# Performance work log

Measured on AMD Instinct MI355X. Metric: run time of the kernel, lower is better.

## Reference

```python
import jax, jax.numpy as jnp
import numpy as np

B, T, D, H = 4, 2048, 1024, 16
DK = D // H

def setup_inputs() -> dict:
    key = jax.random.key(0)
    k1, k2, k3 = jax.random.split(key, 3)
    x = jax.random.normal(k1, (B, T, D), dtype=jnp.float32)
    w_qkv = jax.random.normal(k2, (D, 3 * D), dtype=jnp.float32) * (1.0 / np.sqrt(D))
    w_proj = jax.random.normal(k3, (D, D), dtype=jnp.float32) * (1.0 / np.sqrt(D))
    # additive causal mask: 0 on/below diagonal, -inf above
    neg = jnp.finfo(jnp.float32).min
    attn_mask = jnp.where(jnp.tril(jnp.ones((T, T), dtype=bool)), 0.0, neg)[None, None]
    return {"x": x, "attn_mask": attn_mask, "w_qkv": w_qkv, "w_proj": w_proj}


def reference(x, attn_mask, w_qkv, w_proj):
    Bx, Tx, Dx = x.shape
    qkv = x @ w_qkv                                  # [B,T,3D]
    q, k, v = jnp.split(qkv, 3, axis=-1)
    # [B,T,D] -> [B,H,T,dk]
    def to_heads(t):
        return t.reshape(Bx, Tx, H, DK).transpose(0, 2, 1, 3)
    q, k, v = to_heads(q), to_heads(k), to_heads(v)
    attn = jnp.einsum("bhqd,bhkd->bhqk", q, k) / jnp.sqrt(jnp.float32(DK))
    attn = attn + attn_mask
    attn = jax.nn.softmax(attn, axis=-1)
    out = jnp.einsum("bhqk,bhkd->bhqd", attn, v)     # [B,H,T,dk]
    out = out.transpose(0, 2, 1, 3).reshape(Bx, Tx, Dx)
    return out @ w_proj
```

## Files before the change

kernel.cpp:

```cpp
#include <hip/hip_runtime.h>
#include <hip/hip_bf16.h>
#include <stdint.h>

typedef __bf16 bf16x8 __attribute__((ext_vector_type(8)));
typedef __bf16 bf16x4 __attribute__((ext_vector_type(4)));
typedef float  f32x4  __attribute__((ext_vector_type(4)));

__device__ __forceinline__ void gl_lds16(const void* g, void* l) {
  __builtin_amdgcn_global_load_lds(
      (const __attribute__((address_space(1))) unsigned int*)g,
      (__attribute__((address_space(3))) unsigned int*)l, 16, 0, 0);
}

__global__ __launch_bounds__(256) void prep_kernel(
    const float* __restrict__ x, __bf16* __restrict__ Xb,
    const float* __restrict__ w_qkv, __bf16* __restrict__ wt_qkv,
    const float* __restrict__ w_proj, __bf16* __restrict__ wt_proj) {
  __shared__ __bf16 tile[64][65];
  const int bid = blockIdx.x, t = threadIdx.x;
  if (bid < 4096) {
    const size_t i = ((size_t)bid * 256 + t) * 8;
    float4 v0 = *reinterpret_cast<const float4*>(x + i);
    float4 v1 = *reinterpret_cast<const float4*>(x + i + 4);
    bf16x8 o;
    o[0] = (__bf16)v0.x; o[1] = (__bf16)v0.y; o[2] = (__bf16)v0.z; o[3] = (__bf16)v0.w;
    o[4] = (__bf16)v1.x; o[5] = (__bf16)v1.y; o[6] = (__bf16)v1.z; o[7] = (__bf16)v1.w;
    *reinterpret_cast<bf16x8*>(Xb + i) = o;
    return;
  }
  const float* src; __bf16* dst; int K, N, bx, by;
  if (bid < 4864) {
    int idx = bid - 4096;
    src = w_qkv; dst = wt_qkv; K = 1024; N = 3072;
    bx = idx % 48; by = idx / 48;
  } else {
    int idx = bid - 4864;
    src = w_proj; dst = wt_proj; K = 1024; N = 1024;
    bx = idx & 15; by = idx >> 4;
  }
  const int n0 = bx * 64, k0 = by * 64;
#pragma unroll
  for (int e = 0; e < 16; ++e) {
    int idx = e * 256 + t;
    int kk = idx >> 6, nn = idx & 63;
    tile[nn][kk] = (__bf16)src[(size_t)(k0 + kk) * N + n0 + nn];
  }
  __syncthreads();
#pragma unroll
  for (int e = 0; e < 16; ++e) {
    int idx = e * 256 + t;
    int nn = idx >> 6, kk = idx & 63;
    dst[(size_t)(n0 + nn) * K + k0 + kk] = tile[nn][kk];
  }
}

template <int NFRAG>
__device__ __forceinline__ void gemm_core_1024(
    const __bf16* __restrict__ Ag, const __bf16* __restrict__ Bg,
    int m0, int n0, __bf16* lds, f32x4 (&acc)[8][NFRAG]) {
  constexpr int BUFSZ = 4096 + NFRAG * 2048;
  const int tid = threadIdx.x;
  const int wv = tid >> 6, l = tid & 63, g = l >> 4, lr = l & 15;
  const int sswL = (lr & 3) ^ ((lr >> 2) & 3);

  int arow[2], acol[2], brow[NFRAG], bcol[NFRAG];
#pragma unroll
  for (int e = 0; e < 2; ++e) {
    int c = e * 256 + tid, row = c >> 2, slot = c & 3;
    arow[e] = row;
    acol[e] = (slot ^ ((row & 3) ^ ((row >> 2) & 3))) * 8;
  }
#pragma unroll
  for (int e = 0; e < NFRAG; ++e) {
    int c = e * 256 + tid, row = c >> 2, slot = c & 3;
    brow[e] = row;
    bcol[e] = (slot ^ ((row & 3) ^ ((row >> 2) & 3))) * 8;
  }

  auto STAGE = [&](int bufb, int t) {
    const int kb = t * 32;
#pragma unroll
    for (int e = 0; e < 2; ++e)
      gl_lds16(Ag + (size_t)(m0 + arow[e]) * 1024 + kb + acol[e],
               lds + bufb + (e * 256 + wv * 64) * 8);
#pragma unroll
    for (int e = 0; e < NFRAG; ++e)
      gl_lds16(Bg + (size_t)(n0 + brow[e]) * 1024 + kb + bcol[e],
               lds + bufb + 4096 + (e * 256 + wv * 64) * 8);
  };

  int cur = 0, nx = BUFSZ, nn = 2 * BUFSZ;
  STAGE(cur, 0);
  STAGE(nx, 1);

#pragma unroll 1
  for (int t = 0; t < 32; ++t) {
    if (t < 31) {
      if constexpr (NFRAG == 3) asm volatile("s_waitcnt vmcnt(5)" ::: "memory");
      else                      asm volatile("s_waitcnt vmcnt(4)" ::: "memory");
    } else {
      asm volatile("s_waitcnt vmcnt(0)" ::: "memory");
    }
    __builtin_amdgcn_s_barrier();
    __builtin_amdgcn_sched_barrier(0);
    if (t + 2 < 32) STAGE(nn, t + 2);

    const char* Ab = (const char*)(lds + cur);
    const char* Bb = (const char*)(lds + cur + 4096);
    bf16x8 a[8], b[NFRAG];
#pragma unroll
    for (int mf = 0; mf < 8; ++mf)
      a[mf] = *reinterpret_cast<const bf16x8*>(
          Ab + (mf * 16 + lr) * 64 + ((g ^ sswL) << 4));
#pragma unroll
    for (int nf = 0; nf < NFRAG; ++nf)
      b[nf] = *reinterpret_cast<const bf16x8*>(
          Bb + (wv * NFRAG * 16 + nf * 16 + lr) * 64 + ((g ^ sswL) << 4));
    __builtin_amdgcn_s_setprio(1);
#pragma unroll
    for (int mf = 0; mf < 8; ++mf)
#pragma unroll
      for (int nf = 0; nf < NFRAG; ++nf)
        acc[mf][nf] = __builtin_amdgcn_mfma_f32_16x16x32_bf16(
            a[mf], b[nf], acc[mf][nf], 0, 0, 0);
    __builtin_amdgcn_s_setprio(0);

    int tmp = cur; cur = nx; nx = nn; nn = tmp;
  }
}

__global__ __launch_bounds__(256, 2) void qkv_gemm(
    const __bf16* __restrict__ Xb, const __bf16* __restrict__ WT,
    __bf16* __restrict__ Qb, __bf16* __restrict__ Kb, __bf16* __restrict__ Vb) {
  __shared__ __bf16 lds[30720];
  const int lin = blockIdx.x;
  const int sw = (lin & 7) * 128 + (lin >> 3);
  const int rb = sw >> 4, cb = sw & 15;
  const int m0 = rb * 128, n0 = cb * 192;

  f32x4 acc[8][3] = {};
  gemm_core_1024<3>(Xb, WT, m0, n0, lds, acc);

  const int tid = threadIdx.x, wv = tid >> 6, l = tid & 63, g = l >> 4, lr = l & 15;
#pragma unroll
  for (int mf = 0; mf < 8; ++mf)
#pragma unroll
    for (int nf = 0; nf < 3; ++nf) {
      int m_ = m0 + mf * 16 + g * 4;
      int nb = n0 + wv * 48 + nf * 16;
      int which = nb >> 10, hc = nb & 1023;
      int hh = hc >> 6, dk0 = hc & 63;
      int bbv = m_ >> 11, tt = m_ & 2047;
      if (which == 2) {
        bf16x4 vk;
        vk[0] = (__bf16)acc[mf][nf][0]; vk[1] = (__bf16)acc[mf][nf][1];
        vk[2] = (__bf16)acc[mf][nf][2]; vk[3] = (__bf16)acc[mf][nf][3];
        *reinterpret_cast<bf16x4*>(
            &Vb[((size_t)(bbv * 16 + hh) * 64 + dk0 + lr) * 2048 + tt]) = vk;
      } else if (which == 0) {
#pragma unroll
        for (int j = 0; j < 4; ++j)
          Qb[(((size_t)(bbv * 16 + hh)) * 2048 + tt + j) * 64 + dk0 + lr] =
              (__bf16)(acc[mf][nf][j] * 0.18033688f);
      } else {
#pragma unroll
        for (int j = 0; j < 4; ++j)
          Kb[(((size_t)(bbv * 16 + hh)) * 2048 + tt + j) * 64 + dk0 + lr] =
              (__bf16)acc[mf][nf][j];
      }
    }
}

__global__ __launch_bounds__(256, 2) void proj_gemm(
    const __bf16* __restrict__ A, const __bf16* __restrict__ WT,
    float* __restrict__ Out) {
  __shared__ __bf16 lds[24576];
  const int lin = blockIdx.x;
  const int sw = (lin & 7) * 64 + (lin >> 3);
  const int rb = sw >> 3, cb = sw & 7;
  const int m0 = rb * 128, n0 = cb * 128;

  f32x4 acc[8][2] = {};
  gemm_core_1024<2>(A, WT, m0, n0, lds, acc);

  const int tid = threadIdx.x, wv = tid >> 6, l = tid & 63, g = l >> 4, lr = l & 15;
#pragma unroll
  for (int mf = 0; mf < 8; ++mf)
#pragma unroll
    for (int nf = 0; nf < 2; ++nf) {
      int m_ = m0 + mf * 16 + g * 4;
      int n  = n0 + wv * 32 + nf * 16 + lr;
#pragma unroll
      for (int j = 0; j < 4; ++j)
        Out[(size_t)(m_ + j) * 1024 + n] = acc[mf][nf][j];
    }
}

__global__ __launch_bounds__(256, 2) void attn_kernel(
    const __bf16* __restrict__ Qb, const __bf16* __restrict__ Kb,
    const __bf16* __restrict__ VTb, __bf16* __restrict__ Ob) {
  __shared__ __bf16 Ks[2][4096];
  __shared__ __bf16 Vs[2][4096];
  __shared__ __bf16 PlA[4][1024];
  __shared__ __bf16 PlB[4][1024];
  const int t = threadIdx.x, l = t & 63, w = t >> 6;
  const int g = l >> 4, lr = l & 15;
  const int bid = blockIdx.x;
  const int logical = (bid & 7) * 64 + (bid >> 3);
  const int pj = logical & 7, bh = logical >> 3;
  const int bb = bh >> 4, h = bh & 15;
  const __bf16* Kbase = Kb  + (size_t)bh * 2048 * 64;
  const __bf16* Vbase = VTb + (size_t)bh * 64 * 2048;
  const __bf16* Qbase = Qb  + (size_t)bh * 2048 * 64;
  const int swz = (lr & 7) << 4;

  int cur = 0;
#pragma unroll 1
  for (int phase = 0; phase < 2; ++phase) {
    const int J = phase ? (15 - pj) : pj;
    const int qtA = 2 * J, qtB = 2 * J + 1;
    const int qrowA = J * 128 + w * 16 + lr;
    const int qrowB = qrowA + 64;
    const bf16x8 qfA0 = *reinterpret_cast<const bf16x8*>(Qbase + (size_t)qrowA * 64 + g * 8);
    const bf16x8 qfA1 = *reinterpret_cast<const bf16x8*>(Qbase + (size_t)qrowA * 64 + 32 + g * 8);
    const bf16x8 qfB0 = *reinterpret_cast<const bf16x8*>(Qbase + (size_t)qrowB * 64 + g * 8);
    const bf16x8 qfB1 = *reinterpret_cast<const bf16x8*>(Qbase + (size_t)qrowB * 64 + 32 + g * 8);

    f32x4 otA[4] = {}, otB[4] = {};
    float lsA = 0.f, lsB = 0.f;

#pragma unroll
    for (int rep = 0; rep < 2; ++rep) {
      int c = w * 128 + rep * 64 + l;
      int row = c >> 3, cc = c & 7;
      int pc = (cc ^ (row & 7)) * 8;
      gl_lds16(Kbase + (size_t)row * 64 + pc, &Ks[cur][(w * 128 + rep * 64) * 8]);
      gl_lds16(Vbase + (size_t)row * 2048 + pc, &Vs[cur][(w * 128 + rep * 64) * 8]);
    }
    __syncthreads();

    for (int kt = 0; kt <= qtB; ++kt) {
      const bool aAct = (kt <= qtA);
      if (kt < qtB) {
        const int nv0 = (kt + 1) * 64;
#pragma unroll
        for (int rep = 0; rep < 2; ++rep) {
          int c = w * 128 + rep * 64 + l;
          int row = c >> 3, cc = c & 7;
          int pc = (cc ^ (row & 7)) * 8;
          gl_lds16(Kbase + (size_t)(nv0 + row) * 64 + pc,
                   &Ks[cur ^ 1][(w * 128 + rep * 64) * 8]);
          gl_lds16(Vbase + (size_t)row * 2048 + nv0 + pc,
                   &Vs[cur ^ 1][(w * 128 + rep * 64) * 8]);
        }
      }
      bf16x8 klo[4], khi[4];
#pragma unroll
      for (int nf = 0; nf < 4; ++nf) {
        const char* kr = (const char*)&Ks[cur][(nf * 16 + lr) * 64];
        klo[nf] = *reinterpret_cast<const bf16x8*>(kr + ((g * 16) ^ swz));
        khi[nf] = *reinterpret_cast<const bf16x8*>(kr + ((64 + g * 16) ^ swz));
      }
      f32x4 stA[4], stB[4];
      __builtin_amdgcn_s_setprio(1);
#pragma unroll
      for (int nf = 0; nf < 4; ++nf) {
        f32x4 z = {};
        z = __builtin_amdgcn_mfma_f32_16x16x32_bf16(klo[nf], qfB0, z, 0, 0, 0);
        stB[nf] = __builtin_amdgcn_mfma_f32_16x16x32_bf16(khi[nf], qfB1, z, 0, 0, 0);
      }
      if (aAct) {
#pragma unroll
        for (int nf = 0; nf < 4; ++nf) {
          f32x4 z = {};
          z = __builtin_amdgcn_mfma_f32_16x16x32_bf16(klo[nf], qfA0, z, 0, 0, 0);
          stA[nf] = __builtin_amdgcn_mfma_f32_16x16x32_bf16(khi[nf], qfA1, z, 0, 0, 0);
        }
      }
      __builtin_amdgcn_s_setprio(0);
      if (kt == qtB) {
#pragma unroll
        for (int nf = 0; nf < 4; ++nf)
#pragma unroll
          for (int j = 0; j < 4; ++j)
            if (nf * 16 + g * 4 + j > w * 16 + lr) stB[nf][j] = -INFINITY;
      }
      if (aAct && kt == qtA) {
#pragma unroll
        for (int nf = 0; nf < 4; ++nf)
#pragma unroll
          for (int j = 0; j < 4; ++j)
            if (nf * 16 + g * 4 + j > w * 16 + lr) stA[nf][j] = -INFINITY;
      }
      {
        float rs = 0.f;
        char* prow = (char*)&PlB[w][lr * 64];
#pragma unroll
        for (int nf = 0; nf < 4; ++nf) {
#pragma unroll
          for (int j = 0; j < 4; ++j) {
            float p = __builtin_amdgcn_exp2f(stB[nf][j]);
            stB[nf][j] = p;
            rs += p;
          }
          bf16x4 pk;
          pk[0] = (__bf16)stB[nf][0]; pk[1] = (__bf16)stB[nf][1];
          pk[2] = (__bf16)stB[nf][2]; pk[3] = (__bf16)stB[nf][3];
          *reinterpret_cast<bf16x4*>(prow + ((nf * 32 + g * 8) ^ swz)) = pk;
        }
        lsB += rs;
      }
      if (aAct) {
        float rs = 0.f;
        char* prow = (char*)&PlA[w][lr * 64];
#pragma unroll
        for (int nf = 0; nf < 4; ++nf) {
#pragma unroll
          for (int j = 0; j < 4; ++j) {
            float p = __builtin_amdgcn_exp2f(stA[nf][j]);
            stA[nf][j] = p;
            rs += p;
          }
          bf16x4 pk;
          pk[0] = (__bf16)stA[nf][0]; pk[1] = (__bf16)stA[nf][1];
          pk[2] = (__bf16)stA[nf][2]; pk[3] = (__bf16)stA[nf][3];
          *reinterpret_cast<bf16x4*>(prow + ((nf * 32 + g * 8) ^ swz)) = pk;
        }
        lsA += rs;
      }
      {
        bf16x8 vlo[4], vhi[4];
#pragma unroll
        for (int nf = 0; nf < 4; ++nf) {
          const char* vr = (const char*)&Vs[cur][(nf * 16 + lr) * 64];
          vlo[nf] = *reinterpret_cast<const bf16x8*>(vr + ((g * 16) ^ swz));
          vhi[nf] = *reinterpret_cast<const bf16x8*>(vr + ((64 + g * 16) ^ swz));
        }
        const char* prB = (const char*)&PlB[w][lr * 64];
        bf16x8 pb0 = *reinterpret_cast<const bf16x8*>(prB + ((g * 16) ^ swz));
        bf16x8 pb1 = *reinterpret_cast<const bf16x8*>(prB + ((64 + g * 16) ^ swz));
        __builtin_amdgcn_s_setprio(1);
#pragma unroll
        for (int nf = 0; nf < 4; ++nf) {
          otB[nf] = __builtin_amdgcn_mfma_f32_16x16x32_bf16(vlo[nf], pb0, otB[nf], 0, 0, 0);
          otB[nf] = __builtin_amdgcn_mfma_f32_16x16x32_bf16(vhi[nf], pb1, otB[nf], 0, 0, 0);
        }
        __builtin_amdgcn_s_setprio(0);
        if (aAct) {
          const char* prA = (const char*)&PlA[w][lr * 64];
          bf16x8 pa0 = *reinterpret_cast<const bf16x8*>(prA + ((g * 16) ^ swz));
          bf16x8 pa1 = *reinterpret_cast<const bf16x8*>(prA + ((64 + g * 16) ^ swz));
          __builtin_amdgcn_s_setprio(1);
#pragma unroll
          for (int nf = 0; nf < 4; ++nf) {
            otA[nf] = __builtin_amdgcn_mfma_f32_16x16x32_bf16(vlo[nf], pa0, otA[nf], 0, 0, 0);
            otA[nf] = __builtin_amdgcn_mfma_f32_16x16x32_bf16(vhi[nf], pa1, otA[nf], 0, 0, 0);
          }
          __builtin_amdgcn_s_setprio(0);
        }
      }
      __syncthreads();
      cur ^= 1;
    }

    lsA += __shfl_xor(lsA, 16); lsA += __shfl_xor(lsA, 32);
    lsB += __shfl_xor(lsB, 16); lsB += __shfl_xor(lsB, 32);
    const float rlA = 1.f / lsA, rlB = 1.f / lsB;
#pragma unroll
    for (int nf = 0; nf < 4; ++nf) {
      bf16x4 ok;
      ok[0] = (__bf16)(otA[nf][0] * rlA); ok[1] = (__bf16)(otA[nf][1] * rlA);
      ok[2] = (__bf16)(otA[nf][2] * rlA); ok[3] = (__bf16)(otA[nf][3] * rlA);
      *reinterpret_cast<bf16x4*>(
          &Ob[((size_t)(bb * 2048 + qrowA)) * 1024 + h * 64 + nf * 16 + g * 4]) = ok;
      bf16x4 ok2;
      ok2[0] = (__bf16)(otB[nf][0] * rlB); ok2[1] = (__bf16)(otB[nf][1] * rlB);
      ok2[2] = (__bf16)(otB[nf][2] * rlB); ok2[3] = (__bf16)(otB[nf][3] * rlB);
      *reinterpret_cast<bf16x4*>(
          &Ob[((size_t)(bb * 2048 + qrowB)) * 1024 + h * 64 + nf * 16 + g * 4]) = ok2;
    }
  }
}

extern "C" void kernel_launch(void* const* d_in, const int* in_sizes, int n_in,
                              void* d_out, int out_size, void* d_ws, size_t ws_size,
                              hipStream_t stream) {
  const float* x      = (const float*)d_in[0];
  const float* w_qkv  = (const float*)d_in[2];
  const float* w_proj = (const float*)d_in[3];
  float* out = (float*)d_out;

  char* ws = (char*)d_ws;
  __bf16* wt_qkv  = (__bf16*)(ws);
  __bf16* wt_proj = (__bf16*)(ws + 6291456);
  __bf16* Qb      = (__bf16*)(ws + 8388608);
  __bf16* Kb      = (__bf16*)(ws + 8388608 + 16777216);
  __bf16* VTb     = (__bf16*)(ws + 8388608 + 2 * 16777216);
  __bf16* Ob      = (__bf16*)(ws + 8388608 + 3 * 16777216);
  __bf16* Xb      = Ob;

  prep_kernel<<<5120, 256, 0, stream>>>(x, Xb, w_qkv, wt_qkv, w_proj, wt_proj);
  qkv_gemm<<<1024, 256, 0, stream>>>(Xb, wt_qkv, Qb, Kb, VTb);
  attn_kernel<<<512, 256, 0, stream>>>(Qb, Kb, VTb, Ob);
  proj_gemm<<<512, 256, 0, stream>>>(Ob, wt_proj, out);
}
```

Baseline: 159.6 us.

## Switch QKV and projection GEMMs to 256x256 tiles with 8 waves

Replaces the 128-row GEMM core with a 256x256 block tile computed by 512 threads arranged as 2x4 waves, with a new LDS swizzle and triple buffering. The B-tile prefetch is split to issue between the two MFMA halves, with extra barriers. Larger tiles raise arithmetic intensity and cut global loads per FLOP. The cost is far fewer blocks (384 and 128), one block per CU, and possible load imbalance and lower occupancy.

```diff
diff --git a/kernel.cpp b/kernel.cpp
--- a/kernel.cpp
+++ b/kernel.cpp
@@ -54,142 +54,142 @@
   }
 }
 
-template <int NFRAG>
-__device__ __forceinline__ void gemm_core_1024(
-    const __bf16* __restrict__ Ag, const __bf16* __restrict__ Bg,
-    int m0, int n0, __bf16* lds, f32x4 (&acc)[8][NFRAG]) {
-  constexpr int BUFSZ = 4096 + NFRAG * 2048;
-  const int tid = threadIdx.x;
-  const int wv = tid >> 6, l = tid & 63, g = l >> 4, lr = l & 15;
-  const int sswL = (lr & 3) ^ ((lr >> 2) & 3);
-
-  int arow[2], acol[2], brow[NFRAG], bcol[NFRAG];
-#pragma unroll
-  for (int e = 0; e < 2; ++e) {
-    int c = e * 256 + tid, row = c >> 2, slot = c & 3;
-    arow[e] = row;
-    acol[e] = (slot ^ ((row & 3) ^ ((row >> 2) & 3))) * 8;
-  }
-#pragma unroll
-  for (int e = 0; e < NFRAG; ++e) {
-    int c = e * 256 + tid, row = c >> 2, slot = c & 3;
-    brow[e] = row;
-    bcol[e] = (slot ^ ((row & 3) ^ ((row >> 2) & 3))) * 8;
-  }
-
-  auto STAGE = [&](int bufb, int t) {
-    const int kb = t * 32;
-#pragma unroll
-    for (int e = 0; e < 2; ++e)
-      gl_lds16(Ag + (size_t)(m0 + arow[e]) * 1024 + kb + acol[e],
-               lds + bufb + (e * 256 + wv * 64) * 8);
-#pragma unroll
-    for (int e = 0; e < NFRAG; ++e)
-      gl_lds16(Bg + (size_t)(n0 + brow[e]) * 1024 + kb + bcol[e],
-               lds + bufb + 4096 + (e * 256 + wv * 64) * 8);
-  };
-
-  int cur = 0, nx = BUFSZ, nn = 2 * BUFSZ;
-  STAGE(cur, 0);
-  STAGE(nx, 1);
-
-#pragma unroll 1
-  for (int t = 0; t < 32; ++t) {
-    if (t < 31) {
-      if constexpr (NFRAG == 3) asm volatile("s_waitcnt vmcnt(5)" ::: "memory");
-      else                      asm volatile("s_waitcnt vmcnt(4)" ::: "memory");
-    } else {
-      asm volatile("s_waitcnt vmcnt(0)" ::: "memory");
-    }
-    __builtin_amdgcn_s_barrier();
-    __builtin_amdgcn_sched_barrier(0);
-    if (t + 2 < 32) STAGE(nn, t + 2);
-
-    const char* Ab = (const char*)(lds + cur);
-    const char* Bb = (const char*)(lds + cur + 4096);
-    bf16x8 a[8], b[NFRAG];
-#pragma unroll
-    for (int mf = 0; mf < 8; ++mf)
-      a[mf] = *reinterpret_cast<const bf16x8*>(
-          Ab + (mf * 16 + lr) * 64 + ((g ^ sswL) << 4));
-#pragma unroll
-    for (int nf = 0; nf < NFRAG; ++nf)
-      b[nf] = *reinterpret_cast<const bf16x8*>(
-          Bb + (wv * NFRAG * 16 + nf * 16 + lr) * 64 + ((g ^ sswL) << 4));
-    __builtin_amdgcn_s_setprio(1);
-#pragma unroll
-    for (int mf = 0; mf < 8; ++mf)
-#pragma unroll
-      for (int nf = 0; nf < NFRAG; ++nf)
-        acc[mf][nf] = __builtin_amdgcn_mfma_f32_16x16x32_bf16(
-            a[mf], b[nf], acc[mf][nf], 0, 0, 0);
-    __builtin_amdgcn_s_setprio(0);
-
-    int tmp = cur; cur = nx; nx = nn; nn = tmp;
-  }
-}
-
-__global__ __launch_bounds__(256, 2) void qkv_gemm(
+#define GEMM256_CORE(Ag, Bg, m0, n0, lds, acc)                                  \
+  const int tid = threadIdx.x;                                                  \
+  const int wv = tid >> 6, l = tid & 63, g = l >> 4, lr = l & 15;               \
+  const int wm = wv >> 2, wn = wv & 3;                                          \
+  int srow[2], scol[2];                                                         \
+  _Pragma("unroll")                                                             \
+  for (int e = 0; e < 2; ++e) {                                                 \
+    int c = e * 512 + tid;                                                      \
+    int row = c >> 2, slot = c & 3;                                             \
+    srow[e] = row;                                                              \
+    scol[e] = (slot ^ ((row >> 1) & 3)) * 8;                                    \
+  }                                                                             \
+  const int sdst0 = tid * 8;                                                    \
+  auto STAGE_A = [&](int buf, int t) {                                          \
+    const int kb = t * 32;                                                      \
+    _Pragma("unroll")                                                           \
+    for (int e = 0; e < 2; ++e)                                                 \
+      gl_lds16(Ag + (size_t)(m0 + srow[e]) * 1024 + kb + scol[e],               \
+               lds + buf * 16384 + e * 4096 + sdst0);                           \
+  };                                                                            \
+  auto STAGE_B = [&](int buf, int t) {                                          \
+    const int kb = t * 32;                                                      \
+    _Pragma("unroll")                                                           \
+    for (int e = 0; e < 2; ++e)                                                 \
+      gl_lds16(Bg + (size_t)(n0 + srow[e]) * 1024 + kb + scol[e],               \
+               lds + buf * 16384 + 8192 + e * 4096 + sdst0);                    \
+  };                                                                            \
+  const int swb = (g ^ ((lr >> 1) & 3)) * 8;                                    \
+  const int arow0 = wm * 128 + lr;                                              \
+  const int brow0 = wn * 64 + lr;                                               \
+  STAGE_A(0, 0); STAGE_B(0, 0);                                                 \
+  STAGE_A(1, 1); STAGE_B(1, 1);                                                 \
+  int bt = 0;                                                                   \
+  _Pragma("unroll 1")                                                           \
+  for (int t = 0; t < 32; ++t) {                                                \
+    if (t < 31) asm volatile("s_waitcnt vmcnt(4)" ::: "memory");                \
+    else        asm volatile("s_waitcnt vmcnt(0)" ::: "memory");                \
+    __builtin_amdgcn_s_barrier();                                               \
+    __builtin_amdgcn_sched_barrier(0);                                          \
+    const __bf16* Ab = lds + bt * 16384;                                        \
+    const __bf16* Bb = Ab + 8192;                                               \
+    const int bs = (bt + 2 >= 3) ? (bt - 1) : (bt + 2);                         \
+    bf16x8 a[8], b[4];                                                          \
+    if (t + 2 < 32) STAGE_A(bs, t + 2);                                         \
+    _Pragma("unroll")                                                           \
+    for (int mf = 0; mf < 4; ++mf)                                              \
+      a[mf] = *reinterpret_cast<const bf16x8*>(Ab + (arow0 + mf * 16) * 32 + swb); \
+    _Pragma("unroll")                                                           \
+    for (int nf = 0; nf < 4; ++nf)                                              \
+      b[nf] = *reinterpret_cast<const bf16x8*>(Bb + (brow0 + nf * 16) * 32 + swb); \
+    __builtin_amdgcn_s_barrier();                                               \
+    __builtin_amdgcn_s_setprio(1);                                              \
+    _Pragma("unroll")                                                           \
+    for (int mf = 0; mf < 4; ++mf)                                              \
+      _Pragma("unroll")                                                         \
+      for (int nf = 0; nf < 4; ++nf)                                            \
+        acc[mf][nf] = __builtin_amdgcn_mfma_f32_16x16x32_bf16(                  \
+            a[mf], b[nf], acc[mf][nf], 0, 0, 0);                                \
+    __builtin_amdgcn_s_setprio(0);                                              \
+    __builtin_amdgcn_sched_barrier(0);                                          \
+    if (t + 2 < 32) STAGE_B(bs, t + 2);                                         \
+    _Pragma("unroll")                                                           \
+    for (int mf = 4; mf < 8; ++mf)                                              \
+      a[mf] = *reinterpret_cast<const bf16x8*>(Ab + (arow0 + mf * 16) * 32 + swb); \
+    __builtin_amdgcn_s_barrier();                                               \
+    __builtin_amdgcn_s_setprio(1);                                              \
+    _Pragma("unroll")                                                           \
+    for (int mf = 4; mf < 8; ++mf)                                              \
+      _Pragma("unroll")                                                         \
+      for (int nf = 0; nf < 4; ++nf)                                            \
+        acc[mf][nf] = __builtin_amdgcn_mfma_f32_16x16x32_bf16(                  \
+            a[mf], b[nf], acc[mf][nf], 0, 0, 0);                                \
+    __builtin_amdgcn_s_setprio(0);                                              \
+    __builtin_amdgcn_sched_barrier(0);                                          \
+    bt = (bt + 1 == 3) ? 0 : bt + 1;                                            \
+  }
+
+__global__ __launch_bounds__(512, 1) void qkv_gemm(
     const __bf16* __restrict__ Xb, const __bf16* __restrict__ WT,
     __bf16* __restrict__ Qb, __bf16* __restrict__ Kb, __bf16* __restrict__ Vb) {
-  __shared__ __bf16 lds[30720];
+  __shared__ __bf16 lds[49152];
   const int lin = blockIdx.x;
-  const int sw = (lin & 7) * 128 + (lin >> 3);
-  const int rb = sw >> 4, cb = sw & 15;
-  const int m0 = rb * 128, n0 = cb * 192;
-
-  f32x4 acc[8][3] = {};
-  gemm_core_1024<3>(Xb, WT, m0, n0, lds, acc);
-
-  const int tid = threadIdx.x, wv = tid >> 6, l = tid & 63, g = l >> 4, lr = l & 15;
+  const int sw = (lin & 7) * 48 + (lin >> 3);
+  const int rb = sw / 12, cb = sw % 12;
+  const int m0 = rb * 256, n0 = cb * 256;
+
+  f32x4 acc[8][4] = {};
+  GEMM256_CORE(Xb, WT, m0, n0, lds, acc)
+
+  const int which = cb >> 2;
 #pragma unroll
   for (int mf = 0; mf < 8; ++mf)
 #pragma unroll
-    for (int nf = 0; nf < 3; ++nf) {
-      int m_ = m0 + mf * 16 + g * 4;
-      int nb = n0 + wv * 48 + nf * 16;
-      int which = nb >> 10, hc = nb & 1023;
-      int hh = hc >> 6, dk0 = hc & 63;
+    for (int nf = 0; nf < 4; ++nf) {
+      int m_ = m0 + wm * 128 + mf * 16 + g * 4;
+      int n  = n0 + wn * 64 + nf * 16 + lr;
+      int hc = n & 1023, hh = hc >> 6, dk = hc & 63;
       int bbv = m_ >> 11, tt = m_ & 2047;
       if (which == 2) {
         bf16x4 vk;
         vk[0] = (__bf16)acc[mf][nf][0]; vk[1] = (__bf16)acc[mf][nf][1];
         vk[2] = (__bf16)acc[mf][nf][2]; vk[3] = (__bf16)acc[mf][nf][3];
         *reinterpret_cast<bf16x4*>(
-            &Vb[((size_t)(bbv * 16 + hh) * 64 + dk0 + lr) * 2048 + tt]) = vk;
+            &Vb[((size_t)(bbv * 16 + hh) * 64 + dk) * 2048 + tt]) = vk;
       } else if (which == 0) {
 #pragma unroll
         for (int j = 0; j < 4; ++j)
-          Qb[(((size_t)(bbv * 16 + hh)) * 2048 + tt + j) * 64 + dk0 + lr] =
+          Qb[(((size_t)(bbv * 16 + hh)) * 2048 + tt + j) * 64 + dk] =
               (__bf16)(acc[mf][nf][j] * 0.18033688f);
       } else {
 #pragma unroll
         for (int j = 0; j < 4; ++j)
-          Kb[(((size_t)(bbv * 16 + hh)) * 2048 + tt + j) * 64 + dk0 + lr] =
+          Kb[(((size_t)(bbv * 16 + hh)) * 2048 + tt + j) * 64 + dk] =
               (__bf16)acc[mf][nf][j];
       }
     }
 }
 
-__global__ __launch_bounds__(256, 2) void proj_gemm(
+__global__ __launch_bounds__(512, 1) void proj_gemm(
     const __bf16* __restrict__ A, const __bf16* __restrict__ WT,
     float* __restrict__ Out) {
-  __shared__ __bf16 lds[24576];
+  __shared__ __bf16 lds[49152];
   const int lin = blockIdx.x;
-  const int sw = (lin & 7) * 64 + (lin >> 3);
-  const int rb = sw >> 3, cb = sw & 7;
-  const int m0 = rb * 128, n0 = cb * 128;
-
-  f32x4 acc[8][2] = {};
-  gemm_core_1024<2>(A, WT, m0, n0, lds, acc);
-
-  const int tid = threadIdx.x, wv = tid >> 6, l = tid & 63, g = l >> 4, lr = l & 15;
+  const int sw = (lin & 7) * 16 + (lin >> 3);
+  const int rb = sw >> 2, cb = sw & 3;
+  const int m0 = rb * 256, n0 = cb * 256;
+
+  f32x4 acc[8][4] = {};
+  GEMM256_CORE(A, WT, m0, n0, lds, acc)
+
 #pragma unroll
   for (int mf = 0; mf < 8; ++mf)
 #pragma unroll
-    for (int nf = 0; nf < 2; ++nf) {
-      int m_ = m0 + mf * 16 + g * 4;
-      int n  = n0 + wv * 32 + nf * 16 + lr;
+    for (int nf = 0; nf < 4; ++nf) {
+      int m_ = m0 + wm * 128 + mf * 16 + g * 4;
+      int n  = n0 + wn * 64 + nf * 16 + lr;
 #pragma unroll
       for (int j = 0; j < 4; ++j)
         Out[(size_t)(m_ + j) * 1024 + n] = acc[mf][nf][j];
@@ -400,7 +400,7 @@
   __bf16* Xb      = Ob;
 
   prep_kernel<<<5120, 256, 0, stream>>>(x, Xb, w_qkv, wt_qkv, w_proj, wt_proj);
-  qkv_gemm<<<1024, 256, 0, stream>>>(Xb, wt_qkv, Qb, Kb, VTb);
+  qkv_gemm<<<384, 512, 0, stream>>>(Xb, wt_qkv, Qb, Kb, VTb);
   attn_kernel<<<512, 256, 0, stream>>>(Qb, Kb, VTb, Ob);
-  proj_gemm<<<512, 256, 0, stream>>>(Ob, wt_proj, out);
-}
+  proj_gemm<<<128, 512, 0, stream>>>(Ob, wt_proj, out);
+}
```

New measurement: 170.0 us. 6.5% more time.

## Rewrite QKV GEMM with 256x256 tiles, 8 waves, and interleaved staging

Applied to the files above, without the earlier changes.

The QKV projection GEMM moves from 128x192 tiles with 4 waves to 256x256 tiles with 8 waves (2x4 wave grid) and 384 blocks. Loads are issued half-tile at a time and interleaved with the MFMA phases under a two-buffer LDS scheme with its own XOR swizzle. The aim is more data reuse per LDS byte and fewer global loads. The shared gemm_core read swizzle expression is also changed, which affects proj_gemm and risks a mismatch with how that core stages data if sswL was computed differently.

```diff
diff --git a/kernel.cpp b/kernel.cpp
--- a/kernel.cpp
+++ b/kernel.cpp
@@ -111,11 +111,11 @@
 #pragma unroll
     for (int mf = 0; mf < 8; ++mf)
       a[mf] = *reinterpret_cast<const bf16x8*>(
-          Ab + (mf * 16 + lr) * 64 + ((g ^ sswL) << 4));
+          Ab + (mf * 16 + lr) * 64 + (((lr & 3) ^ ((lr >> 2) & 3) ^ g) << 4));
 #pragma unroll
     for (int nf = 0; nf < NFRAG; ++nf)
       b[nf] = *reinterpret_cast<const bf16x8*>(
-          Bb + (wv * NFRAG * 16 + nf * 16 + lr) * 64 + ((g ^ sswL) << 4));
+          Bb + (wv * NFRAG * 16 + nf * 16 + lr) * 64 + (((lr & 3) ^ ((lr >> 2) & 3) ^ g) << 4));
     __builtin_amdgcn_s_setprio(1);
 #pragma unroll
     for (int mf = 0; mf < 8; ++mf)
@@ -129,43 +129,108 @@
   }
 }
 
-__global__ __launch_bounds__(256, 2) void qkv_gemm(
+__global__ __launch_bounds__(512, 2) void qkv_gemm(
     const __bf16* __restrict__ Xb, const __bf16* __restrict__ WT,
     __bf16* __restrict__ Qb, __bf16* __restrict__ Kb, __bf16* __restrict__ Vb) {
-  __shared__ __bf16 lds[30720];
+  __shared__ __bf16 lds[32768];
+  const int tid = threadIdx.x;
+  const int wv = tid >> 6, l = tid & 63, g = l >> 4, lr = l & 15;
+  const int wm = wv >> 2, wn = wv & 3;
   const int lin = blockIdx.x;
-  const int sw = (lin & 7) * 128 + (lin >> 3);
-  const int rb = sw >> 4, cb = sw & 15;
-  const int m0 = rb * 128, n0 = cb * 192;
-
-  f32x4 acc[8][3] = {};
-  gemm_core_1024<3>(Xb, WT, m0, n0, lds, acc);
-
-  const int tid = threadIdx.x, wv = tid >> 6, l = tid & 63, g = l >> 4, lr = l & 15;
+  const int sw = (lin & 7) * 48 + (lin >> 3);
+  const int rb = sw / 12, cb = sw % 12;
+  const int m0 = rb * 256, n0 = cb * 256;
+
+  const int strow = tid >> 2;
+  const int stcol = ((tid & 3) ^ ((strow >> 1) & 3)) * 8;
+
+  auto STAGE2 = [&](int tile, int isB) {
+    if (tile >= 32) return;
+    const __bf16* G = isB ? WT : Xb;
+    const int gr0 = isB ? n0 : m0;
+    __bf16* dst = lds + (isB ? 16384 : 0) + (tile & 1) * 8192;
+#pragma unroll
+    for (int h = 0; h < 2; ++h)
+      gl_lds16(G + (size_t)(gr0 + h * 128 + strow) * 1024 + tile * 32 + stcol,
+               dst + h * 4096 + tid * 8);
+  };
+
+  f32x4 acc[8][4] = {};
+
+  STAGE2(0, 1); STAGE2(0, 0); STAGE2(1, 1);
+  asm volatile("s_waitcnt vmcnt(2)" ::: "memory");
+  __builtin_amdgcn_s_barrier();
+
+  bf16x8 b[4];
+#pragma unroll 1
+  for (int i = 0; i < 16; ++i) {
+    const int t0 = 2 * i;
+#pragma unroll
+    for (int p = 0; p < 4; ++p) {
+      const int kt = p >> 1, mh = p & 1;
+      bf16x8 a[4];
+#pragma unroll
+      for (int m4 = 0; m4 < 4; ++m4) {
+        int r = wm * 128 + (mh * 4 + m4) * 16 + lr;
+        int sl = (g ^ ((r >> 1) & 3)) * 8;
+        a[m4] = *reinterpret_cast<const bf16x8*>(lds + kt * 8192 + r * 32 + sl);
+      }
+      if (mh == 0) {
+#pragma unroll
+        for (int nf = 0; nf < 4; ++nf) {
+          int r = wn * 64 + nf * 16 + lr;
+          int sl = (g ^ ((r >> 1) & 3)) * 8;
+          b[nf] = *reinterpret_cast<const bf16x8*>(lds + 16384 + kt * 8192 + r * 32 + sl);
+        }
+      }
+      if (p == 0) STAGE2(t0 + 1, 0);
+      if (p == 1) STAGE2(t0 + 2, 1);
+      if (p == 2) STAGE2(t0 + 2, 0);
+      if (p == 3) STAGE2(t0 + 3, 1);
+      __builtin_amdgcn_s_barrier();
+      asm volatile("s_waitcnt lgkmcnt(0)" ::: "memory");
+      __builtin_amdgcn_sched_barrier(0);
+      __builtin_amdgcn_s_setprio(1);
+#pragma unroll
+      for (int m4 = 0; m4 < 4; ++m4)
+#pragma unroll
+        for (int nf = 0; nf < 4; ++nf)
+          acc[mh * 4 + m4][nf] = __builtin_amdgcn_mfma_f32_16x16x32_bf16(
+              a[m4], b[nf], acc[mh * 4 + m4][nf], 0, 0, 0);
+      __builtin_amdgcn_s_setprio(0);
+      __builtin_amdgcn_sched_barrier(0);
+      if (p == 1 || p == 3) {
+        if (i < 15) asm volatile("s_waitcnt vmcnt(2)" ::: "memory");
+        else        asm volatile("s_waitcnt vmcnt(0)" ::: "memory");
+      }
+      __builtin_amdgcn_s_barrier();
+    }
+  }
+
+  const int which = cb >> 2;
 #pragma unroll
   for (int mf = 0; mf < 8; ++mf)
 #pragma unroll
-    for (int nf = 0; nf < 3; ++nf) {
-      int m_ = m0 + mf * 16 + g * 4;
-      int nb = n0 + wv * 48 + nf * 16;
-      int which = nb >> 10, hc = nb & 1023;
-      int hh = hc >> 6, dk0 = hc & 63;
+    for (int nf = 0; nf < 4; ++nf) {
+      int m_ = m0 + wm * 128 + mf * 16 + g * 4;
+      int n  = n0 + wn * 64 + nf * 16 + lr;
+      int hc = n & 1023, hh = hc >> 6, dk = hc & 63;
       int bbv = m_ >> 11, tt = m_ & 2047;
       if (which == 2) {
         bf16x4 vk;
         vk[0] = (__bf16)acc[mf][nf][0]; vk[1] = (__bf16)acc[mf][nf][1];
         vk[2] = (__bf16)acc[mf][nf][2]; vk[3] = (__bf16)acc[mf][nf][3];
         *reinterpret_cast<bf16x4*>(
-            &Vb[((size_t)(bbv * 16 + hh) * 64 + dk0 + lr) * 2048 + tt]) = vk;
+            &Vb[((size_t)(bbv * 16 + hh) * 64 + dk) * 2048 + tt]) = vk;
       } else if (which == 0) {
 #pragma unroll
         for (int j = 0; j < 4; ++j)
-          Qb[(((size_t)(bbv * 16 + hh)) * 2048 + tt + j) * 64 + dk0 + lr] =
+          Qb[(((size_t)(bbv * 16 + hh)) * 2048 + tt + j) * 64 + dk] =
               (__bf16)(acc[mf][nf][j] * 0.18033688f);
       } else {
 #pragma unroll
         for (int j = 0; j < 4; ++j)
-          Kb[(((size_t)(bbv * 16 + hh)) * 2048 + tt + j) * 64 + dk0 + lr] =
+          Kb[(((size_t)(bbv * 16 + hh)) * 2048 + tt + j) * 64 + dk] =
               (__bf16)acc[mf][nf][j];
       }
     }
@@ -400,7 +465,7 @@
   __bf16* Xb      = Ob;
 
   prep_kernel<<<5120, 256, 0, stream>>>(x, Xb, w_qkv, wt_qkv, w_proj, wt_proj);
-  qkv_gemm<<<1024, 256, 0, stream>>>(Xb, wt_qkv, Qb, Kb, VTb);
+  qkv_gemm<<<384, 512, 0, stream>>>(Xb, wt_qkv, Qb, Kb, VTb);
   attn_kernel<<<512, 256, 0, stream>>>(Qb, Kb, VTb, Ob);
   proj_gemm<<<512, 256, 0, stream>>>(Ob, wt_proj, out);
 }
```

Measured after the change: 161.9 us. No clear change (+1.4%).

## Use 2x2 wave tiling with 128x128 tiles and four-stage LDS pipeline in GEMMs

Applied to the files above, without the earlier changes.

Replaces the GEMM core with a uniform 128x128 block tile in which the four waves form a 2x2 grid, each owning a 64x64 sub-tile, instead of every wave reading all 128 A rows. The loads now cycle through four LDS buffers three stages ahead, and fragment reads are issued before the next stage's global loads. This is meant to cut per-wave LDS fragment reads and hide more global latency. The QKV GEMM moves from 128x192 tiles to 128x128 (1536 blocks). The cost is more LDS per block (64 KB), which may limit occupancy.

```diff
diff --git a/kernel.cpp b/kernel.cpp
--- a/kernel.cpp
+++ b/kernel.cpp
@@ -54,118 +54,114 @@
   }
 }
 
-template <int NFRAG>
-__device__ __forceinline__ void gemm_core_1024(
+__device__ __forceinline__ void gemm128_core(
     const __bf16* __restrict__ Ag, const __bf16* __restrict__ Bg,
-    int m0, int n0, __bf16* lds, f32x4 (&acc)[8][NFRAG]) {
-  constexpr int BUFSZ = 4096 + NFRAG * 2048;
+    int m0, int n0, __bf16* lds, f32x4 (&acc)[4][4]) {
   const int tid = threadIdx.x;
   const int wv = tid >> 6, l = tid & 63, g = l >> 4, lr = l & 15;
-  const int sswL = (lr & 3) ^ ((lr >> 2) & 3);
-
-  int arow[2], acol[2], brow[NFRAG], bcol[NFRAG];
+  const int wm = wv >> 1, wn = wv & 1;
+
+  int srow[2], scolG[2];
 #pragma unroll
   for (int e = 0; e < 2; ++e) {
-    int c = e * 256 + tid, row = c >> 2, slot = c & 3;
-    arow[e] = row;
-    acol[e] = (slot ^ ((row & 3) ^ ((row >> 2) & 3))) * 8;
-  }
-#pragma unroll
-  for (int e = 0; e < NFRAG; ++e) {
-    int c = e * 256 + tid, row = c >> 2, slot = c & 3;
-    brow[e] = row;
-    bcol[e] = (slot ^ ((row & 3) ^ ((row >> 2) & 3))) * 8;
-  }
-
-  auto STAGE = [&](int bufb, int t) {
-    const int kb = t * 32;
-#pragma unroll
-    for (int e = 0; e < 2; ++e)
-      gl_lds16(Ag + (size_t)(m0 + arow[e]) * 1024 + kb + acol[e],
-               lds + bufb + (e * 256 + wv * 64) * 8);
-#pragma unroll
-    for (int e = 0; e < NFRAG; ++e)
-      gl_lds16(Bg + (size_t)(n0 + brow[e]) * 1024 + kb + bcol[e],
-               lds + bufb + 4096 + (e * 256 + wv * 64) * 8);
+    int linear = e * 256 + tid;
+    int row = linear >> 2, slotP = linear & 3;
+    srow[e] = row;
+    scolG[e] = (slotP ^ (row & 3) ^ ((row >> 2) & 3)) * 8;
+  }
+
+  auto STAGE = [&](int t) {
+    if (t >= 32) return;
+    const int bufO = (t & 3) * 8192;
+    const int kg = t * 32;
+#pragma unroll
+    for (int e = 0; e < 2; ++e) {
+      gl_lds16(Ag + (size_t)(m0 + srow[e]) * 1024 + kg + scolG[e],
+               lds + bufO + (e * 256 + tid) * 8);
+      gl_lds16(Bg + (size_t)(n0 + srow[e]) * 1024 + kg + scolG[e],
+               lds + bufO + 4096 + (e * 256 + tid) * 8);
+    }
   };
 
-  int cur = 0, nx = BUFSZ, nn = 2 * BUFSZ;
-  STAGE(cur, 0);
-  STAGE(nx, 1);
+  const int sl8 = (g ^ (lr & 3) ^ ((lr >> 2) & 3)) * 8;
+  const int arow0 = wm * 64 + lr;
+  const int brow0 = wn * 64 + lr;
+
+  STAGE(0); STAGE(1); STAGE(2);
 
 #pragma unroll 1
   for (int t = 0; t < 32; ++t) {
-    if (t < 31) {
-      if constexpr (NFRAG == 3) asm volatile("s_waitcnt vmcnt(5)" ::: "memory");
-      else                      asm volatile("s_waitcnt vmcnt(4)" ::: "memory");
-    } else {
-      asm volatile("s_waitcnt vmcnt(0)" ::: "memory");
-    }
+    if (t < 30)       asm volatile("s_waitcnt vmcnt(8)" ::: "memory");
+    else if (t == 30) asm volatile("s_waitcnt vmcnt(4)" ::: "memory");
+    else              asm volatile("s_waitcnt vmcnt(0)" ::: "memory");
     __builtin_amdgcn_s_barrier();
     __builtin_amdgcn_sched_barrier(0);
-    if (t + 2 < 32) STAGE(nn, t + 2);
-
-    const char* Ab = (const char*)(lds + cur);
-    const char* Bb = (const char*)(lds + cur + 4096);
-    bf16x8 a[8], b[NFRAG];
-#pragma unroll
-    for (int mf = 0; mf < 8; ++mf)
-      a[mf] = *reinterpret_cast<const bf16x8*>(
-          Ab + (mf * 16 + lr) * 64 + ((g ^ sswL) << 4));
-#pragma unroll
-    for (int nf = 0; nf < NFRAG; ++nf)
-      b[nf] = *reinterpret_cast<const bf16x8*>(
-          Bb + (wv * NFRAG * 16 + nf * 16 + lr) * 64 + ((g ^ sswL) << 4));
+
+    const __bf16* buf = lds + (t & 3) * 8192;
+    bf16x8 a[4], b[4];
+#pragma unroll
+    for (int mf = 0; mf < 4; ++mf)
+      a[mf] = *reinterpret_cast<const bf16x8*>(buf + (arow0 + mf * 16) * 32 + sl8);
+#pragma unroll
+    for (int nf = 0; nf < 4; ++nf)
+      b[nf] = *reinterpret_cast<const bf16x8*>(buf + 4096 + (brow0 + nf * 16) * 32 + sl8);
+
+    STAGE(t + 3);
+
+    asm volatile("s_waitcnt lgkmcnt(0)" ::: "memory");
+    __builtin_amdgcn_sched_barrier(0);
     __builtin_amdgcn_s_setprio(1);
 #pragma unroll
-    for (int mf = 0; mf < 8; ++mf)
-#pragma unroll
-      for (int nf = 0; nf < NFRAG; ++nf)
+    for (int mf = 0; mf < 4; ++mf)
+#pragma unroll
+      for (int nf = 0; nf < 4; ++nf)
         acc[mf][nf] = __builtin_amdgcn_mfma_f32_16x16x32_bf16(
             a[mf], b[nf], acc[mf][nf], 0, 0, 0);
     __builtin_amdgcn_s_setprio(0);
-
-    int tmp = cur; cur = nx; nx = nn; nn = tmp;
+    __builtin_amdgcn_sched_barrier(0);
   }
 }
 
 __global__ __launch_bounds__(256, 2) void qkv_gemm(
     const __bf16* __restrict__ Xb, const __bf16* __restrict__ WT,
     __bf16* __restrict__ Qb, __bf16* __restrict__ Kb, __bf16* __restrict__ Vb) {
-  __shared__ __bf16 lds[30720];
+  __shared__ __bf16 lds[32768];
   const int lin = blockIdx.x;
-  const int sw = (lin & 7) * 128 + (lin >> 3);
-  const int rb = sw >> 4, cb = sw & 15;
-  const int m0 = rb * 128, n0 = cb * 192;
-
-  f32x4 acc[8][3] = {};
-  gemm_core_1024<3>(Xb, WT, m0, n0, lds, acc);
-
-  const int tid = threadIdx.x, wv = tid >> 6, l = tid & 63, g = l >> 4, lr = l & 15;
-#pragma unroll
-  for (int mf = 0; mf < 8; ++mf)
-#pragma unroll
-    for (int nf = 0; nf < 3; ++nf) {
-      int m_ = m0 + mf * 16 + g * 4;
-      int nb = n0 + wv * 48 + nf * 16;
-      int which = nb >> 10, hc = nb & 1023;
-      int hh = hc >> 6, dk0 = hc & 63;
+  const int sw = (lin & 7) * 192 + (lin >> 3);
+  const int rb = sw / 24, cb = sw % 24;
+  const int m0 = rb * 128, n0 = cb * 128;
+
+  f32x4 acc[4][4] = {};
+  gemm128_core(Xb, WT, m0, n0, lds, acc);
+
+  const int tid = threadIdx.x;
+  const int wv = tid >> 6, l = tid & 63, g = l >> 4, lr = l & 15;
+  const int wm = wv >> 1, wn = wv & 1;
+  const int which = cb >> 3;
+
+#pragma unroll
+  for (int mf = 0; mf < 4; ++mf)
+#pragma unroll
+    for (int nf = 0; nf < 4; ++nf) {
+      int m_ = m0 + wm * 64 + mf * 16 + g * 4;
+      int n  = n0 + wn * 64 + nf * 16 + lr;
+      int hc = n & 1023, hh = hc >> 6, dk = hc & 63;
       int bbv = m_ >> 11, tt = m_ & 2047;
       if (which == 2) {
         bf16x4 vk;
         vk[0] = (__bf16)acc[mf][nf][0]; vk[1] = (__bf16)acc[mf][nf][1];
         vk[2] = (__bf16)acc[mf][nf][2]; vk[3] = (__bf16)acc[mf][nf][3];
         *reinterpret_cast<bf16x4*>(
-            &Vb[((size_t)(bbv * 16 + hh) * 64 + dk0 + lr) * 2048 + tt]) = vk;
+            &Vb[((size_t)(bbv * 16 + hh) * 64 + dk) * 2048 + tt]) = vk;
       } else if (which == 0) {
 #pragma unroll
         for (int j = 0; j < 4; ++j)
-          Qb[(((size_t)(bbv * 16 + hh)) * 2048 + tt + j) * 64 + dk0 + lr] =
+          Qb[(((size_t)(bbv * 16 + hh)) * 2048 + tt + j) * 64 + dk] =
               (__bf16)(acc[mf][nf][j] * 0.18033688f);
       } else {
 #pragma unroll
         for (int j = 0; j < 4; ++j)
-          Kb[(((size_t)(bbv * 16 + hh)) * 2048 + tt + j) * 64 + dk0 + lr] =
+          Kb[(((size_t)(bbv * 16 + hh)) * 2048 + tt + j) * 64 + dk] =
               (__bf16)acc[mf][nf][j];
       }
     }
@@ -174,22 +170,24 @@
 __global__ __launch_bounds__(256, 2) void proj_gemm(
     const __bf16* __restrict__ A, const __bf16* __restrict__ WT,
     float* __restrict__ Out) {
-  __shared__ __bf16 lds[24576];
+  __shared__ __bf16 lds[32768];
   const int lin = blockIdx.x;
   const int sw = (lin & 7) * 64 + (lin >> 3);
   const int rb = sw >> 3, cb = sw & 7;
   const int m0 = rb * 128, n0 = cb * 128;
 
-  f32x4 acc[8][2] = {};
-  gemm_core_1024<2>(A, WT, m0, n0, lds, acc);
-
-  const int tid = threadIdx.x, wv = tid >> 6, l = tid & 63, g = l >> 4, lr = l & 15;
-#pragma unroll
-  for (int mf = 0; mf < 8; ++mf)
-#pragma unroll
-    for (int nf = 0; nf < 2; ++nf) {
-      int m_ = m0 + mf * 16 + g * 4;
-      int n  = n0 + wv * 32 + nf * 16 + lr;
+  f32x4 acc[4][4] = {};
+  gemm128_core(A, WT, m0, n0, lds, acc);
+
+  const int tid = threadIdx.x;
+  const int wv = tid >> 6, l = tid & 63, g = l >> 4, lr = l & 15;
+  const int wm = wv >> 1, wn = wv & 1;
+#pragma unroll
+  for (int mf = 0; mf < 4; ++mf)
+#pragma unroll
+    for (int nf = 0; nf < 4; ++nf) {
+      int m_ = m0 + wm * 64 + mf * 16 + g * 4;
+      int n  = n0 + wn * 64 + nf * 16 + lr;
 #pragma unroll
       for (int j = 0; j < 4; ++j)
         Out[(size_t)(m_ + j) * 1024 + n] = acc[mf][nf][j];
@@ -400,7 +398,7 @@
   __bf16* Xb      = Ob;
 
   prep_kernel<<<5120, 256, 0, stream>>>(x, Xb, w_qkv, wt_qkv, w_proj, wt_proj);
-  qkv_gemm<<<1024, 256, 0, stream>>>(Xb, wt_qkv, Qb, Kb, VTb);
+  qkv_gemm<<<1536, 256, 0, stream>>>(Xb, wt_qkv, Qb, Kb, VTb);
   attn_kernel<<<512, 256, 0, stream>>>(Qb, Kb, VTb, Ob);
   proj_gemm<<<512, 256, 0, stream>>>(Ob, wt_proj, out);
 }
```

Measured after the change: 165.7 us. 1.04x slower.
